# Optimization experiments

Hardware: AMD Instinct MI355X
Metric: run time of the kernel (lower is better)

## Reference

```python
import math
import jax, jax.numpy as jnp
import numpy as np

B, S, DM, H, KH = 2, 2048, 1024, 16, 4
HD = DM // H          # 64
N_REP = H // KH       # 4
ROPE_THETA = 10000.0


def setup_inputs() -> dict:
    key = jax.random.key(0)
    ks = jax.random.split(key, 5)
    x = jax.random.normal(ks[0], (B, S, DM), dtype=jnp.float32)
    wq = jax.random.normal(ks[1], (H * HD, DM), dtype=jnp.float32) * 0.02
    wk = jax.random.normal(ks[2], (KH * HD, DM), dtype=jnp.float32) * 0.02
    wv = jax.random.normal(ks[3], (KH * HD, DM), dtype=jnp.float32) * 0.02
    wo = jax.random.normal(ks[4], (DM, H * HD), dtype=jnp.float32) * 0.02
    # freqs_cis = exp(i * t * theta^(-2j/d)) represented as cos/sin, shape [S, HD//2]
    inv_freq = 1.0 / (ROPE_THETA ** (jnp.arange(0, HD, 2, dtype=jnp.float32) / HD))
    angles = jnp.arange(S, dtype=jnp.float32)[:, None] * inv_freq[None, :]
    return {
        'x': x, 'wq': wq, 'wk': wk, 'wv': wv, 'wo': wo,
        'freqs_cos': jnp.cos(angles), 'freqs_sin': jnp.sin(angles),
    }


def _rope(t, cos, sin):
    # t: [B, S, h, HD]; pairs (even, odd) rotated as complex mul
    tr = t.reshape(*t.shape[:-1], HD // 2, 2)
    xr, xi = tr[..., 0], tr[..., 1]
    c = cos[None, :, None, :]  # [1, S, 1, HD//2]
    s = sin[None, :, None, :]
    out = jnp.stack([xr * c - xi * s, xr * s + xi * c], axis=-1)
    return out.reshape(t.shape)


def reference(x, wq, wk, wv, wo, freqs_cos, freqs_sin):
    b, s, _ = x.shape
    xq = (x @ wq.T).reshape(b, s, H, HD)
    xk = (x @ wk.T).reshape(b, s, KH, HD)
    xv = (x @ wv.T).reshape(b, s, KH, HD)
    xq = _rope(xq, freqs_cos, freqs_sin)
    xk = _rope(xk, freqs_cos, freqs_sin)
    # [B, h, S, HD]
    xq = xq.transpose(0, 2, 1, 3)
    xk = xk.transpose(0, 2, 1, 3)
    xv = xv.transpose(0, 2, 1, 3)
    # GQA: repeat_interleave kv heads to match query heads
    xk = jnp.repeat(xk, N_REP, axis=1)
    xv = jnp.repeat(xv, N_REP, axis=1)
    scale = 1.0 / math.sqrt(HD)
    scores = jnp.einsum('bhqd,bhkd->bhqk', xq, xk) * scale
    causal = jnp.tril(jnp.ones((s, s), dtype=bool))
    scores = jnp.where(causal[None, None], scores, jnp.finfo(scores.dtype).min)
    attn = jax.nn.softmax(scores, axis=-1)
    out = jnp.einsum('bhqk,bhkd->bhqd', attn, xv)
    out = out.transpose(0, 2, 1, 3).reshape(b, s, H * HD)
    return out @ wo.T
```

## Files before the change

### kernel.cpp

```cpp
#include <hip/hip_runtime.h>
#include <hip/hip_bf16.h>
#include <type_traits>

#define B_ 2
#define S_ 2048
#define DM_ 1024
#define H_ 16
#define KH_ 4
#define HD_ 64
#define NREP_ 4
#define QKV_LD 1536
#define CLOG 0.1803368801111244f
#define FIXM 8.0f

typedef float f32x4 __attribute__((ext_vector_type(4)));
typedef float f32x16 __attribute__((ext_vector_type(16)));
typedef short s16x8 __attribute__((ext_vector_type(8)));
typedef unsigned int u32x2 __attribute__((ext_vector_type(2)));

static __device__ __forceinline__ float bf2f(unsigned short u) {
  union { unsigned int u; float f; } x; x.u = ((unsigned int)u) << 16; return x.f;
}
static __device__ __forceinline__ unsigned short f2bf(float f) {
  union { float f; unsigned int u; } x; x.f = f;
  unsigned int r = (x.u + 0x7fffu + ((x.u >> 16) & 1u)) >> 16;
  return (unsigned short)r;
}
static __device__ __forceinline__ unsigned int cvtpk_bf16(float lo, float hi) {
  unsigned int r;
  asm("v_cvt_pk_bf16_f32 %0, %1, %2" : "=v"(r) : "v"(lo), "v"(hi));
  return r;
}
static __device__ __forceinline__ float fexp2(float x) {
  float r;
  asm("v_exp_f32 %0, %1" : "=v"(r) : "v"(x));
  return r;
}

__device__ __forceinline__ void gload_lds16(const unsigned short* g, unsigned short* l) {
  __builtin_amdgcn_global_load_lds(
      (const __attribute__((address_space(1))) unsigned int*)g,
      (__attribute__((address_space(3))) unsigned int*)l, 16, 0, 0);
}

__global__ void cvt_all_k(const float* __restrict__ x,
                          const float* __restrict__ wq, const float* __restrict__ wk,
                          const float* __restrict__ wv, const float* __restrict__ wo,
                          unsigned short* __restrict__ xb,
                          unsigned short* __restrict__ wqkv, unsigned short* __restrict__ wob) {
  int i = (blockIdx.x * 256 + threadIdx.x) * 4;
  const float* src; unsigned short* dst; int off;
  if (i < 4194304)      { src = x;  dst = xb;              off = i; }
  else if (i < 5242880) { src = wq; dst = wqkv;            off = i - 4194304; }
  else if (i < 5505024) { src = wk; dst = wqkv + 1048576;  off = i - 5242880; }
  else if (i < 5767168) { src = wv; dst = wqkv + 1310720;  off = i - 5505024; }
  else                  { src = wo; dst = wob;             off = i - 5767168; }
  float4 v = *(const float4*)(src + off);
  ushort4 o;
  o.x = f2bf(v.x); o.y = f2bf(v.y); o.z = f2bf(v.z); o.w = f2bf(v.w);
  *(ushort4*)(dst + off) = o;
}

#define BM 128
#define BN 128
#define BK 32

template <typename OT, bool ROPE>
__global__ __launch_bounds__(256) void gemm_bt(const unsigned short* __restrict__ A,
                                               const unsigned short* __restrict__ Bw,
                                               OT* __restrict__ C,
                                               const float* __restrict__ fc,
                                               const float* __restrict__ fs,
                                               int M, int N, int K) {
  __shared__ unsigned short lds_a[BM * BK];
  __shared__ unsigned short lds_b[BN * BK];
  const int tid = threadIdx.x;
  const int wave = tid >> 6, lane = tid & 63;
  const int lr = lane & 15, lg = lane >> 4;
  const int m0 = blockIdx.y * BM, n0 = blockIdx.x * BN;
  const int wr = wave >> 1, wc = wave & 1;

  f32x4 acc[4][4] = {};

  for (int k0 = 0; k0 < K; k0 += BK) {
    #pragma unroll
    for (int i = 0; i < 2; ++i) {
      int cbase = i * 256 + wave * 64;
      int c = cbase + lane;
      int row = c >> 2, col = (c & 3) << 3;
      gload_lds16(A + (size_t)(m0 + row) * K + k0 + col, &lds_a[cbase * 8]);
      gload_lds16(Bw + (size_t)(n0 + row) * K + k0 + col, &lds_b[cbase * 8]);
    }
    __syncthreads();
    s16x8 af[4], bfr[4];
    #pragma unroll
    for (int mi = 0; mi < 4; ++mi)
      af[mi] = *(const s16x8*)&lds_a[(wr * 64 + mi * 16 + lr) * BK + lg * 8];
    #pragma unroll
    for (int ni = 0; ni < 4; ++ni)
      bfr[ni] = *(const s16x8*)&lds_b[(wc * 64 + ni * 16 + lr) * BK + lg * 8];
    #pragma unroll
    for (int mi = 0; mi < 4; ++mi) {
      #pragma unroll
      for (int ni = 0; ni < 4; ++ni)
        acc[mi][ni] = __builtin_amdgcn_mfma_f32_16x16x32_bf16(af[mi], bfr[ni], acc[mi][ni], 0, 0, 0);
    }
    __syncthreads();
  }
  #pragma unroll
  for (int mi = 0; mi < 4; ++mi) {
    #pragma unroll
    for (int ni = 0; ni < 4; ++ni) {
      const int colbase = n0 + wc * 64 + ni * 16;
      const bool doRope = ROPE && (colbase < 1280);
      const int fi = ((colbase & 63) + lr) >> 1;
      #pragma unroll
      for (int r = 0; r < 4; ++r) {
        int row = m0 + wr * 64 + mi * 16 + lg * 4 + r;
        float v = acc[mi][ni][r];
        if (doRope) {
          float nb = __shfl_xor(v, 1);
          int s = row & (S_ - 1);
          float cs = fc[s * 32 + fi], sn = fs[s * 32 + fi];
          float t = nb * sn;
          v = (lr & 1) ? fmaf(v, cs, t) : fmaf(v, cs, -t);
        }
        int col = colbase + lr;
        if constexpr (std::is_same<OT, unsigned short>::value)
          C[(size_t)row * N + col] = f2bf(v);
        else
          C[(size_t)row * N + col] = v;
      }
    }
  }
}

__global__ void kvpack_k(const unsigned short* __restrict__ qkv,
                         unsigned short* __restrict__ kp, unsigned short* __restrict__ vp) {
  int idx = blockIdx.x * 256 + threadIdx.x;
  int lane = idx & 63;
  int f  = (idx >> 6) & 3;
  int t  = (idx >> 8) & 63;
  int p  = idx >> 14;
  int b = p >> 2, kh = p & 3;
  int ql = lane & 31, hi = lane >> 5;
  {
    int s = t * 32 + ql;
    int d0 = f * 16 + hi * 8;
    const unsigned short* src = qkv + (size_t)(b * S_ + s) * QKV_LD + 1024 + kh * HD_ + d0;
    *(s16x8*)(kp + (size_t)idx * 8) = *(const s16x8*)src;
  }
  {
    int d = (f >> 1) * 32 + ql;
    int kv0 = t * 32 + (f & 1) * 16 + hi * 8;
    const unsigned short* src = qkv + (size_t)(b * S_ + kv0) * QKV_LD + 1280 + kh * HD_ + d;
    s16x8 o;
    #pragma unroll
    for (int e = 0; e < 8; ++e) o[e] = (short)src[(size_t)e * QKV_LD];
    *(s16x8*)(vp + (size_t)idx * 8) = o;
  }
}

__global__ __launch_bounds__(256, 3) void attn_fwd9(const unsigned short* __restrict__ qkv,
                                                    const unsigned short* __restrict__ kp,
                                                    const unsigned short* __restrict__ vp,
                                                    unsigned short* __restrict__ ob) {
  __shared__ float mbuf[2][64][34];
  const int tid = threadIdx.x;
  const int wave = tid >> 6, lane = tid & 63;
  const int ql = lane & 31;
  const int hi = lane >> 5;
  const int bi = blockIdx.x;
  const int xcd = bi & 7;
  const int b = xcd >> 2, kh = xcd & 3;
  const int j = bi >> 3;
  const int h = kh * NREP_ + (j & 3);
  const int bt = j >> 2;

  int c, t0, t1;
  int sW1buf = -1, sM1buf = -1;
  bool sW2 = false, sM2 = false, doOut;
  if (bt < 32) {
    c = 63 - bt;
    int T = c + 1;
    t0 = (wave * T) >> 2; t1 = ((wave + 1) * T) >> 2;
    sW1buf = (wave == 1) ? 0 : (wave == 3) ? 1 : -1;
    sM1buf = (wave == 0) ? 0 : (wave == 2) ? 1 : -1;
    sW2 = (wave == 2); sM2 = (wave == 0);
    doOut = (wave == 0);
  } else if (bt < 40) {
    int bb2 = bt - 32;
    c = (wave < 2) ? (16 + bb2) : (31 - bb2);
    int T = c + 1, Th = T >> 1;
    if ((wave & 1) == 0) { t0 = 0;  t1 = Th; } else { t0 = Th; t1 = T; }
    sW1buf = (wave == 1) ? 0 : (wave == 3) ? 1 : -1;
    sM1buf = (wave == 0) ? 0 : (wave == 2) ? 1 : -1;
    doOut = (wave == 0) || (wave == 2);
  } else {
    c = (bt - 40) * 4 + wave;
    t0 = 0; t1 = c + 1;
    doOut = true;
  }
  const int q = c * 32 + ql;

  const unsigned short* qrow = qkv + (size_t)(b * S_ + q) * QKV_LD + h * HD_;
  s16x8 qf[4];
  #pragma unroll
  for (int ks = 0; ks < 4; ++ks)
    qf[ks] = *(const s16x8*)(qrow + ks * 16 + hi * 8);

  const unsigned short* kpt = kp + ((size_t)(b * KH_ + kh) << 17) + lane * 8;
  const unsigned short* vpt = vp + ((size_t)(b * KH_ + kh) << 17) + lane * 8;

  f32x16 oT0 = {};
  f32x16 oT1 = {};
  float l = 0.f;

  s16x8 ka[4], va[4], kb2[4], vb2[4];

#define LOADKV(T, KK, VV) do { \
    const unsigned short* kp_ = kpt + ((size_t)(T) << 11); \
    KK[0] = *(const s16x8*)(kp_);        KK[1] = *(const s16x8*)(kp_ + 512); \
    KK[2] = *(const s16x8*)(kp_ + 1024); KK[3] = *(const s16x8*)(kp_ + 1536); \
    const unsigned short* vp_ = vpt + ((size_t)(T) << 11); \
    VV[0] = *(const s16x8*)(vp_);        VV[1] = *(const s16x8*)(vp_ + 512); \
    VV[2] = *(const s16x8*)(vp_ + 1024); VV[3] = *(const s16x8*)(vp_ + 1536); \
  } while (0)

  auto body = [&](s16x8 (&KK)[4], s16x8 (&VV)[4], bool diag) __attribute__((always_inline)) {
    f32x16 st = {};
    __builtin_amdgcn_s_setprio(1);
    st = __builtin_amdgcn_mfma_f32_32x32x16_bf16(KK[0], qf[0], st, 0, 0, 0);
    st = __builtin_amdgcn_mfma_f32_32x32x16_bf16(KK[1], qf[1], st, 0, 0, 0);
    st = __builtin_amdgcn_mfma_f32_32x32x16_bf16(KK[2], qf[2], st, 0, 0, 0);
    st = __builtin_amdgcn_mfma_f32_32x32x16_bf16(KK[3], qf[3], st, 0, 0, 0);
    __builtin_amdgcn_s_setprio(0);
    if (diag) {
      #pragma unroll
      for (int r = 0; r < 16; ++r)
        if (((r & 3) + 8 * (r >> 2) + 4 * hi) > ql) st[r] = -1e30f;
    }
    float pr[16];
    #pragma unroll
    for (int r = 0; r < 16; ++r) pr[r] = fexp2(fmaf(st[r], CLOG, -FIXM));
    float s0 = (pr[0] + pr[1]) + (pr[2] + pr[3]);
    float s1 = (pr[4] + pr[5]) + (pr[6] + pr[7]);
    float s2 = (pr[8] + pr[9]) + (pr[10] + pr[11]);
    float s3 = (pr[12] + pr[13]) + (pr[14] + pr[15]);
    l += (s0 + s1) + (s2 + s3);
    #pragma unroll
    for (int ksv = 0; ksv < 2; ++ksv) {
      unsigned int a01 = cvtpk_bf16(pr[ksv * 8 + 0], pr[ksv * 8 + 1]);
      unsigned int a23 = cvtpk_bf16(pr[ksv * 8 + 2], pr[ksv * 8 + 3]);
      unsigned int b45 = cvtpk_bf16(pr[ksv * 8 + 4], pr[ksv * 8 + 5]);
      unsigned int b67 = cvtpk_bf16(pr[ksv * 8 + 6], pr[ksv * 8 + 7]);
      asm volatile("v_permlane32_swap_b32 %0, %1" : "+v"(a01), "+v"(b45));
      asm volatile("v_permlane32_swap_b32 %0, %1" : "+v"(a23), "+v"(b67));
      union { s16x8 v; unsigned int w[4]; } pb;
      pb.w[0] = a01; pb.w[1] = a23; pb.w[2] = b45; pb.w[3] = b67;
      __builtin_amdgcn_s_setprio(1);
      oT0 = __builtin_amdgcn_mfma_f32_32x32x16_bf16(VV[ksv], pb.v, oT0, 0, 0, 0);
      oT1 = __builtin_amdgcn_mfma_f32_32x32x16_bf16(VV[2 + ksv], pb.v, oT1, 0, 0, 0);
      __builtin_amdgcn_s_setprio(0);
    }
  };

  LOADKV(t0, ka, va);
  int t = t0;
  while (t + 1 < t1) {
    LOADKV(t + 1, kb2, vb2);
    body(ka, va, t == c);
    ++t;
    if (t + 1 < t1) LOADKV(t + 1, ka, va);
    body(kb2, vb2, t == c);
    ++t;
  }
  if (t < t1) body(ka, va, t == c);
#undef LOADKV

#define WRITEP(BUF) do { float* mp_ = &mbuf[BUF][lane][0]; \
    _Pragma("unroll") for (int r = 0; r < 16; ++r) { mp_[r] = oT0[r]; mp_[16 + r] = oT1[r]; } \
    mp_[32] = l; } while (0)
#define MERGEP(BUF) do { float* mp_ = &mbuf[BUF][lane][0]; \
    l += mp_[32]; \
    _Pragma("unroll") for (int r = 0; r < 16; ++r) { \
      oT0[r] += mp_[r]; \
      oT1[r] += mp_[16 + r]; } } while (0)

  __syncthreads();
  if (sW1buf >= 0) WRITEP(sW1buf);
  __syncthreads();
  if (sM1buf >= 0) MERGEP(sM1buf);
  __syncthreads();
  if (sW2) WRITEP(0);
  __syncthreads();
  if (sM2) MERGEP(0);
#undef WRITEP
#undef MERGEP

  if (doOut) {
    float l_tot = l + __shfl_xor(l, 32);
    float invl = 1.0f / l_tot;
    unsigned short* orow = ob + (size_t)(b * S_ + q) * DM_ + h * HD_;
    #pragma unroll
    for (int dblk = 0; dblk < 2; ++dblk) {
      #pragma unroll
      for (int g = 0; g < 4; ++g) {
        float e0 = (dblk ? oT1[4 * g + 0] : oT0[4 * g + 0]) * invl;
        float e1 = (dblk ? oT1[4 * g + 1] : oT0[4 * g + 1]) * invl;
        float e2 = (dblk ? oT1[4 * g + 2] : oT0[4 * g + 2]) * invl;
        float e3 = (dblk ? oT1[4 * g + 3] : oT0[4 * g + 3]) * invl;
        u32x2 w;
        w.x = cvtpk_bf16(e0, e1);
        w.y = cvtpk_bf16(e2, e3);
        *(u32x2*)(orow + dblk * 32 + g * 8 + 4 * hi) = w;
      }
    }
  }
}

extern "C" void kernel_launch(void* const* d_in, const int* in_sizes, int n_in,
                              void* d_out, int out_size, void* d_ws, size_t ws_size,
                              hipStream_t stream) {
  const float* x  = (const float*)d_in[0];
  const float* wq = (const float*)d_in[1];
  const float* wk = (const float*)d_in[2];
  const float* wv = (const float*)d_in[3];
  const float* wo = (const float*)d_in[4];
  const float* fc = (const float*)d_in[5];
  const float* fs = (const float*)d_in[6];
  float* out = (float*)d_out;

  const size_t nX    = (size_t)B_ * S_ * DM_;
  const size_t nWQKV = (size_t)QKV_LD * DM_;
  const size_t nWO   = (size_t)DM_ * DM_;
  const size_t nQKV  = (size_t)B_ * S_ * QKV_LD;
  const size_t nKV   = (size_t)B_ * S_ * KH_ * HD_;

  unsigned short* xb    = (unsigned short*)d_ws;
  unsigned short* wqkv  = xb + nX;
  unsigned short* wob   = wqkv + nWQKV;
  unsigned short* qkv   = wob + nWO;
  unsigned short* kpk   = qkv + nQKV;
  unsigned short* vpk   = kpk + nKV;
  unsigned short* a_buf = vpk + nKV;

  const int M = B_ * S_;
  dim3 blk(256);

  cvt_all_k<<<6656, blk, 0, stream>>>(x, wq, wk, wv, wo, xb, wqkv, wob);

  gemm_bt<unsigned short, true><<<dim3(QKV_LD / BN, M / BM), blk, 0, stream>>>(
      xb, wqkv, qkv, fc, fs, M, QKV_LD, DM_);

  kvpack_k<<<512, blk, 0, stream>>>(qkv, kpk, vpk);

  attn_fwd9<<<1408, blk, 0, stream>>>(qkv, kpk, vpk, a_buf);

  gemm_bt<float, false><<<dim3(DM_ / BN, M / BM), blk, 0, stream>>>(
      a_buf, wob, out, nullptr, nullptr, M, DM_, DM_);
}
```

Before: 113.4 us.

## Move RoPE into kvpack and attention Q load; widen GEMM to 512 threads

RoPE leaves the QKV GEMM epilogue. K rotation now happens in the kvpack kernel and Q rotation when the attention kernel loads its query fragments, reading cos/sin as float4. The GEMM is simplified and now runs 8 waves per 128x128 tile (512 threads, 4x2 MFMA tiles per wave), so each thread issues a single global-to-LDS load per k step. This removes the shuffles and scattered cos/sin loads from the GEMM epilogue and halves per-wave accumulator registers. The cost is extra rotation work in attention blocks, where several blocks redundantly rotate the same Q rows, and the rotation now runs on bf16-rounded values instead of the fp32 accumulator.

```diff
diff --git a/kernel.cpp b/kernel.cpp
--- a/kernel.cpp
+++ b/kernel.cpp
@@ -65,12 +65,10 @@
 #define BN 128
 #define BK 32
 
-template <typename OT, bool ROPE>
-__global__ __launch_bounds__(256) void gemm_bt(const unsigned short* __restrict__ A,
+template <typename OT>
+__global__ __launch_bounds__(512) void gemm_bt(const unsigned short* __restrict__ A,
                                                const unsigned short* __restrict__ Bw,
                                                OT* __restrict__ C,
-                                               const float* __restrict__ fc,
-                                               const float* __restrict__ fs,
                                                int M, int N, int K) {
   __shared__ unsigned short lds_a[BM * BK];
   __shared__ unsigned short lds_b[BN * BK];
@@ -78,31 +76,27 @@
   const int wave = tid >> 6, lane = tid & 63;
   const int lr = lane & 15, lg = lane >> 4;
   const int m0 = blockIdx.y * BM, n0 = blockIdx.x * BN;
-  const int wr = wave >> 1, wc = wave & 1;
-
-  f32x4 acc[4][4] = {};
+  const int wr = wave >> 2, wc = wave & 3;
+
+  f32x4 acc[4][2] = {};
+
+  const int srow = tid >> 2, scol = (tid & 3) << 3;
 
   for (int k0 = 0; k0 < K; k0 += BK) {
-    #pragma unroll
-    for (int i = 0; i < 2; ++i) {
-      int cbase = i * 256 + wave * 64;
-      int c = cbase + lane;
-      int row = c >> 2, col = (c & 3) << 3;
-      gload_lds16(A + (size_t)(m0 + row) * K + k0 + col, &lds_a[cbase * 8]);
-      gload_lds16(Bw + (size_t)(n0 + row) * K + k0 + col, &lds_b[cbase * 8]);
-    }
+    gload_lds16(A + (size_t)(m0 + srow) * K + k0 + scol, &lds_a[tid * 8]);
+    gload_lds16(Bw + (size_t)(n0 + srow) * K + k0 + scol, &lds_b[tid * 8]);
     __syncthreads();
-    s16x8 af[4], bfr[4];
+    s16x8 af[4], bfr[2];
     #pragma unroll
     for (int mi = 0; mi < 4; ++mi)
       af[mi] = *(const s16x8*)&lds_a[(wr * 64 + mi * 16 + lr) * BK + lg * 8];
     #pragma unroll
-    for (int ni = 0; ni < 4; ++ni)
-      bfr[ni] = *(const s16x8*)&lds_b[(wc * 64 + ni * 16 + lr) * BK + lg * 8];
+    for (int ni = 0; ni < 2; ++ni)
+      bfr[ni] = *(const s16x8*)&lds_b[(wc * 32 + ni * 16 + lr) * BK + lg * 8];
     #pragma unroll
     for (int mi = 0; mi < 4; ++mi) {
       #pragma unroll
-      for (int ni = 0; ni < 4; ++ni)
+      for (int ni = 0; ni < 2; ++ni)
         acc[mi][ni] = __builtin_amdgcn_mfma_f32_16x16x32_bf16(af[mi], bfr[ni], acc[mi][ni], 0, 0, 0);
     }
     __syncthreads();
@@ -110,32 +104,22 @@
   #pragma unroll
   for (int mi = 0; mi < 4; ++mi) {
     #pragma unroll
-    for (int ni = 0; ni < 4; ++ni) {
-      const int colbase = n0 + wc * 64 + ni * 16;
-      const bool doRope = ROPE && (colbase < 1280);
-      const int fi = ((colbase & 63) + lr) >> 1;
+    for (int ni = 0; ni < 2; ++ni) {
       #pragma unroll
       for (int r = 0; r < 4; ++r) {
         int row = m0 + wr * 64 + mi * 16 + lg * 4 + r;
-        float v = acc[mi][ni][r];
-        if (doRope) {
-          float nb = __shfl_xor(v, 1);
-          int s = row & (S_ - 1);
-          float cs = fc[s * 32 + fi], sn = fs[s * 32 + fi];
-          float t = nb * sn;
-          v = (lr & 1) ? fmaf(v, cs, t) : fmaf(v, cs, -t);
-        }
-        int col = colbase + lr;
+        int col = n0 + wc * 32 + ni * 16 + lr;
         if constexpr (std::is_same<OT, unsigned short>::value)
-          C[(size_t)row * N + col] = f2bf(v);
+          C[(size_t)row * N + col] = f2bf(acc[mi][ni][r]);
         else
-          C[(size_t)row * N + col] = v;
+          C[(size_t)row * N + col] = acc[mi][ni][r];
       }
     }
   }
 }
 
 __global__ void kvpack_k(const unsigned short* __restrict__ qkv,
+                         const float* __restrict__ fc, const float* __restrict__ fs,
                          unsigned short* __restrict__ kp, unsigned short* __restrict__ vp) {
   int idx = blockIdx.x * 256 + threadIdx.x;
   int lane = idx & 63;
@@ -148,7 +132,20 @@
     int s = t * 32 + ql;
     int d0 = f * 16 + hi * 8;
     const unsigned short* src = qkv + (size_t)(b * S_ + s) * QKV_LD + 1024 + kh * HD_ + d0;
-    *(s16x8*)(kp + (size_t)idx * 8) = *(const s16x8*)src;
+    s16x8 v = *(const s16x8*)src;
+    int i0 = d0 >> 1;
+    float4 c4 = *(const float4*)(fc + s * 32 + i0);
+    float4 s4 = *(const float4*)(fs + s * 32 + i0);
+    float cc[4] = {c4.x, c4.y, c4.z, c4.w};
+    float ss[4] = {s4.x, s4.y, s4.z, s4.w};
+    union { s16x8 v; unsigned int w[4]; } o;
+    #pragma unroll
+    for (int e = 0; e < 4; ++e) {
+      float xr = bf2f((unsigned short)v[2 * e]);
+      float xi = bf2f((unsigned short)v[2 * e + 1]);
+      o.w[e] = cvtpk_bf16(xr * cc[e] - xi * ss[e], xr * ss[e] + xi * cc[e]);
+    }
+    *(s16x8*)(kp + (size_t)idx * 8) = o.v;
   }
   {
     int d = (f >> 1) * 32 + ql;
@@ -161,10 +158,12 @@
   }
 }
 
-__global__ __launch_bounds__(256, 3) void attn_fwd9(const unsigned short* __restrict__ qkv,
-                                                    const unsigned short* __restrict__ kp,
-                                                    const unsigned short* __restrict__ vp,
-                                                    unsigned short* __restrict__ ob) {
+__global__ __launch_bounds__(256, 3) void attn_fwd10(const unsigned short* __restrict__ qkv,
+                                                     const unsigned short* __restrict__ kp,
+                                                     const unsigned short* __restrict__ vp,
+                                                     const float* __restrict__ fc,
+                                                     const float* __restrict__ fs,
+                                                     unsigned short* __restrict__ ob) {
   __shared__ float mbuf[2][64][34];
   const int tid = threadIdx.x;
   const int wave = tid >> 6, lane = tid & 63;
@@ -206,8 +205,22 @@
   const unsigned short* qrow = qkv + (size_t)(b * S_ + q) * QKV_LD + h * HD_;
   s16x8 qf[4];
   #pragma unroll
-  for (int ks = 0; ks < 4; ++ks)
-    qf[ks] = *(const s16x8*)(qrow + ks * 16 + hi * 8);
+  for (int ks = 0; ks < 4; ++ks) {
+    s16x8 v = *(const s16x8*)(qrow + ks * 16 + hi * 8);
+    int i0 = ks * 8 + hi * 4;
+    float4 c4 = *(const float4*)(fc + q * 32 + i0);
+    float4 s4 = *(const float4*)(fs + q * 32 + i0);
+    float cc[4] = {c4.x, c4.y, c4.z, c4.w};
+    float ss[4] = {s4.x, s4.y, s4.z, s4.w};
+    union { s16x8 v; unsigned int w[4]; } o;
+    #pragma unroll
+    for (int e = 0; e < 4; ++e) {
+      float xr = bf2f((unsigned short)v[2 * e]);
+      float xi = bf2f((unsigned short)v[2 * e + 1]);
+      o.w[e] = cvtpk_bf16(xr * cc[e] - xi * ss[e], xr * ss[e] + xi * cc[e]);
+    }
+    qf[ks] = o.v;
+  }
 
   const unsigned short* kpt = kp + ((size_t)(b * KH_ + kh) << 17) + lane * 8;
   const unsigned short* vpt = vp + ((size_t)(b * KH_ + kh) << 17) + lane * 8;
@@ -346,17 +359,16 @@
   unsigned short* a_buf = vpk + nKV;
 
   const int M = B_ * S_;
-  dim3 blk(256);
-
-  cvt_all_k<<<6656, blk, 0, stream>>>(x, wq, wk, wv, wo, xb, wqkv, wob);
-
-  gemm_bt<unsigned short, true><<<dim3(QKV_LD / BN, M / BM), blk, 0, stream>>>(
-      xb, wqkv, qkv, fc, fs, M, QKV_LD, DM_);
-
-  kvpack_k<<<512, blk, 0, stream>>>(qkv, kpk, vpk);
-
-  attn_fwd9<<<1408, blk, 0, stream>>>(qkv, kpk, vpk, a_buf);
-
-  gemm_bt<float, false><<<dim3(DM_ / BN, M / BM), blk, 0, stream>>>(
-      a_buf, wob, out, nullptr, nullptr, M, DM_, DM_);
-}
+
+  cvt_all_k<<<6656, 256, 0, stream>>>(x, wq, wk, wv, wo, xb, wqkv, wob);
+
+  gemm_bt<unsigned short><<<dim3(QKV_LD / BN, M / BM), 512, 0, stream>>>(
+      xb, wqkv, qkv, M, QKV_LD, DM_);
+
+  kvpack_k<<<512, 256, 0, stream>>>(qkv, fc, fs, kpk, vpk);
+
+  attn_fwd10<<<1408, 256, 0, stream>>>(qkv, kpk, vpk, fc, fs, a_buf);
+
+  gemm_bt<float><<<dim3(DM_ / BN, M / BM), 512, 0, stream>>>(
+      a_buf, wob, out, M, DM_, DM_);
+}
```

Measured after the change: 98.92 us. 1.15x faster.
